# Kernel tuning notes

Measured on AMD Instinct MI355X. Metric: run time of the kernel, lower is better.

Reference implementation:

```python
import jax, jax.numpy as jnp
import numpy as np

N = 100000
M = 20000
NNZ = 1000000
D_IN = 128
D_OUT = 128


def setup_inputs() -> dict:
    key = jax.random.key(0)
    ks = jax.random.split(key, 6)
    return {
        "node_features": jax.random.normal(ks[0], (N, D_IN), dtype=jnp.float32),
        "data": jax.random.uniform(ks[1], (NNZ,), dtype=jnp.float32),
        "W": jax.random.normal(ks[2], (D_OUT, D_IN), dtype=jnp.float32) / np.sqrt(D_IN),
        "b": jax.random.normal(ks[3], (D_OUT,), dtype=jnp.float32),
        "v_idx": jax.random.randint(ks[4], (NNZ,), 0, N, dtype=jnp.int32),
        "e_idx": jax.random.randint(ks[5], (NNZ,), 0, M, dtype=jnp.int32),
        "n": N,
        "m": M,
    }


def reference(node_features, data, W, b, v_idx, e_idx, n, m):
    # Linear projection (eqx.nn.Linear: y = W @ x + b, vmapped over nodes)
    x = node_features @ W.T + b  # [n, d_out]

    # Degree normalization terms
    d_e = jax.ops.segment_sum(data, e_idx, num_segments=m)  # [m]
    d_v = jax.ops.segment_sum(data, v_idx, num_segments=n)  # [n]
    d_e_inv = jnp.where(d_e > 0, 1.0 / d_e, 0.0)
    d_v_inv = jnp.where(d_v > 0, 1.0 / d_v, 0.0)

    # vertex -> edge: H.T @ x via gather-scale-scatter
    e = jax.ops.segment_sum(x[v_idx] * data[:, None], e_idx, num_segments=m)  # [m, d_out]
    e = e * d_e_inv[:, None]

    # edge -> vertex: H @ e via gather-scale-scatter
    out = jax.ops.segment_sum(e[e_idx] * data[:, None], v_idx, num_segments=n)  # [n, d_out]
    out = out * d_v_inv[:, None]
    return out
```

## Files before the change

kernel.cpp:

```cpp
#include <hip/hip_runtime.h>

#define DF  128
#define NB  128
#define ME  20000
#define EW  10000
#define VW  16667
#define VP  3
#define VSPAN (2 * VW)

typedef float f32x2 __attribute__((ext_vector_type(2)));

__device__ __forceinline__ unsigned bf16rne(float f) {
    unsigned u = __float_as_uint(f);
    return (u + 0x7fffu + ((u >> 16) & 1u)) >> 16;
}

__device__ __forceinline__ unsigned w15enc(float f) {
    unsigned bits = __float_as_uint(f);
    unsigned r = (bits + 0xFFFu + ((bits >> 13) & 1u)) >> 13;
    return (r > (96u << 10)) ? (r - (96u << 10)) : 0u;
}
__device__ __forceinline__ float w15dec(unsigned w) {
    return w ? __uint_as_float((w + (96u << 10)) << 13) : 0.f;
}

#if __has_builtin(__builtin_amdgcn_fdot2_f32_bf16)
typedef __bf16 bf16x2 __attribute__((ext_vector_type(2)));
__device__ __forceinline__ float dot2bf(unsigned a, unsigned b, float c) {
    return __builtin_amdgcn_fdot2_f32_bf16(
        __builtin_bit_cast(bf16x2, a), __builtin_bit_cast(bf16x2, b), c, false);
}
#else
__device__ __forceinline__ float dot2bf(unsigned a, unsigned b, float c) {
    c += __uint_as_float(a << 16) * __uint_as_float(b << 16);
    c += __uint_as_float(a & 0xffff0000u) * __uint_as_float(b & 0xffff0000u);
    return c;
}
#endif

__global__ __launch_bounds__(256) void hist_lds(
    const int* __restrict__ vi, const int* __restrict__ ei,
    unsigned short* __restrict__ rankE, unsigned short* __restrict__ rankV,
    unsigned* __restrict__ bhE, unsigned* __restrict__ bhV, int nnz, int epb)
{
    __shared__ unsigned lh[VW];
    int b = blockIdx.x;
    int lo = b * epb;
    int hi = min(nnz, lo + epb);
    int iters = epb >> 10;

    for (int w = threadIdx.x; w < EW; w += 256) lh[w] = 0;
    __syncthreads();
    for (int it = 0; it < iters; ++it) {
        int i = lo + (it * 256 + threadIdx.x) * 4;
        if (i + 4 <= hi) {
            int4 e4 = *(const int4*)(ei + i);
            int ee[4] = {e4.x, e4.y, e4.z, e4.w};
            unsigned short r[4];
            #pragma unroll
            for (int q = 0; q < 4; ++q) {
                int sh = (ee[q] & 1) * 16;
                unsigned ret = atomicAdd(&lh[ee[q] >> 1], 1u << sh);
                r[q] = (unsigned short)((ret >> sh) & 0xffffu);
            }
            *(ushort4*)(rankE + i) = ushort4{r[0], r[1], r[2], r[3]};
        } else {
            for (int j = i; j < hi; ++j) {
                int e = ei[j]; int sh = (e & 1) * 16;
                unsigned ret = atomicAdd(&lh[e >> 1], 1u << sh);
                rankE[j] = (unsigned short)((ret >> sh) & 0xffffu);
            }
        }
    }
    __syncthreads();
    for (int w = threadIdx.x; w < EW; w += 256)
        bhE[(size_t)b * EW + w] = lh[w];

    for (int p = 0; p < VP; ++p) {
        int vbase = p * VSPAN;
        __syncthreads();
        for (int w = threadIdx.x; w < VW; w += 256) lh[w] = 0;
        __syncthreads();
        for (int it = 0; it < iters; ++it) {
            int i = lo + (it * 256 + threadIdx.x) * 4;
            if (i + 4 <= hi) {
                int4 v4 = *(const int4*)(vi + i);
                int vv[4] = {v4.x, v4.y, v4.z, v4.w};
                #pragma unroll
                for (int q = 0; q < 4; ++q) {
                    int d = vv[q] - vbase;
                    if (d >= 0 && d < VSPAN) {
                        int sh = (d & 1) * 16;
                        unsigned ret = atomicAdd(&lh[d >> 1], 1u << sh);
                        rankV[i + q] = (unsigned short)((ret >> sh) & 0xffffu);
                    }
                }
            } else {
                for (int j = i; j < hi; ++j) {
                    int d = vi[j] - vbase;
                    if (d >= 0 && d < VSPAN) {
                        int sh = (d & 1) * 16;
                        unsigned ret = atomicAdd(&lh[d >> 1], 1u << sh);
                        rankV[j] = (unsigned short)((ret >> sh) & 0xffffu);
                    }
                }
            }
        }
        __syncthreads();
        for (int w = threadIdx.x; w < VW; w += 256)
            bhV[(size_t)b * (VP * VW) + p * VW + w] = lh[w];
    }
}

__global__ __launch_bounds__(256) void scan_cols_conv(
    unsigned* __restrict__ bhE, unsigned* __restrict__ bhV,
    int* __restrict__ totE, int* __restrict__ totV,
    const float* __restrict__ nf, const float* __restrict__ W,
    unsigned* __restrict__ nfh, unsigned* __restrict__ wp, int n, int n64)
{
    int tid = blockIdx.x * 256 + threadIdx.x;
    if (tid < EW) {
        unsigned run0 = 0, run1 = 0;
        #pragma unroll 4
        for (int b = 0; b < NB; ++b) {
            unsigned w = bhE[(size_t)b * EW + tid];
            bhE[(size_t)b * EW + tid] = run0 | (run1 << 16);
            run0 += w & 0xffffu; run1 += w >> 16;
        }
        totE[2 * tid] = (int)run0;
        totE[2 * tid + 1] = (int)run1;
    } else if (tid < EW + VP * VW) {
        int w = tid - EW;
        unsigned run0 = 0, run1 = 0;
        #pragma unroll 4
        for (int b = 0; b < NB; ++b) {
            unsigned x = bhV[(size_t)b * (VP * VW) + w];
            bhV[(size_t)b * (VP * VW) + w] = run0 | (run1 << 16);
            run0 += x & 0xffffu; run1 += x >> 16;
        }
        int p = w / VW, wi = w - p * VW;
        int k0 = p * VSPAN + 2 * wi;
        if (k0 < n) totV[k0] = (int)run0;
        if (k0 + 1 < n) totV[k0 + 1] = (int)run1;
    }
    int nth = gridDim.x * 256;
    const float2* __restrict__ in2 = (const float2*)nf;
    for (int i = tid; i < n64; i += nth) {
        float2 f = in2[i];
        nfh[i] = bf16rne(f.x) | (bf16rne(f.y) << 16);
    }
    if (tid < DF * 64) {
        int j = tid >> 6, k2 = tid & 63;
        float2 f = ((const float2*)W)[tid];
        wp[k2 * DF + j] = bf16rne(f.x) | (bf16rne(f.y) << 16);
    }
}

__global__ __launch_bounds__(256) void scan_k1(
    const int* __restrict__ totE, const int* __restrict__ totV,
    int* __restrict__ bsum, int m, int len)
{
    __shared__ int s[256];
    int tid = threadIdx.x;
    int base = blockIdx.x * 2048 + tid * 8;
    int t = 0;
    #pragma unroll
    for (int i = 0; i < 8; ++i) {
        int idx = base + i;
        if (idx < len) t += (idx < m) ? totE[idx] : totV[idx - m];
    }
    s[tid] = t; __syncthreads();
    for (int d = 128; d > 0; d >>= 1) {
        if (tid < d) s[tid] += s[tid + d];
        __syncthreads();
    }
    if (tid == 0) bsum[blockIdx.x] = s[0];
}

__global__ __launch_bounds__(256) void scan_k2(int* __restrict__ bsum, int nb)
{
    __shared__ int s[256];
    int t = threadIdx.x;
    int v = (t < nb) ? bsum[t] : 0;
    s[t] = v; __syncthreads();
    for (int d = 1; d < 256; d <<= 1) {
        int u = (t >= d) ? s[t - d] : 0;
        __syncthreads();
        s[t] += u;
        __syncthreads();
    }
    if (t < nb) bsum[t] = s[t] - v;
}

__global__ __launch_bounds__(256) void scan_k3(
    const int* __restrict__ totE, const int* __restrict__ totV,
    const int* __restrict__ bsum, int* __restrict__ seg, int m, int len)
{
    __shared__ int s[256];
    int tid = threadIdx.x;
    int base = blockIdx.x * 2048 + tid * 8;
    int v[8]; int t = 0;
    #pragma unroll
    for (int i = 0; i < 8; ++i) {
        int idx = base + i;
        v[i] = (idx < len) ? ((idx < m) ? totE[idx] : totV[idx - m]) : 0;
        t += v[i];
    }
    s[tid] = t; __syncthreads();
    for (int d = 1; d < 256; d <<= 1) {
        int u = (tid >= d) ? s[tid - d] : 0;
        __syncthreads();
        s[tid] += u;
        __syncthreads();
    }
    int run = bsum[blockIdx.x] + (s[tid] - t);
    #pragma unroll
    for (int i = 0; i < 8; ++i) {
        int idx = base + i;
        if (idx < len) { seg[idx] = run; run += v[i]; }
    }
}

__global__ __launch_bounds__(256) void place_kernel(
    const int* __restrict__ vi, const int* __restrict__ ei,
    const float* __restrict__ data,
    const unsigned short* __restrict__ rankE,
    const unsigned short* __restrict__ rankV,
    const int* __restrict__ seg,
    const unsigned* __restrict__ bhE, const unsigned* __restrict__ bhV,
    unsigned* __restrict__ pair, int nnz, int m, int epb)
{
    int base = (blockIdx.x * 256 + threadIdx.x) * 4;
    if (base + 4 <= nnz) {
        int bH = base / epb;
        const unsigned* __restrict__ be = bhE + (size_t)bH * EW;
        const unsigned* __restrict__ bv = bhV + (size_t)bH * (VP * VW);
        int4 e4 = *(const int4*)(ei + base);
        int4 v4 = *(const int4*)(vi + base);
        ushort4 re4 = *(const ushort4*)(rankE + base);
        ushort4 rv4 = *(const ushort4*)(rankV + base);
        float4 d4 = *(const float4*)(data + base);
        int ee[4] = {e4.x, e4.y, e4.z, e4.w};
        int vv[4] = {v4.x, v4.y, v4.z, v4.w};
        unsigned short rre[4] = {re4.x, re4.y, re4.z, re4.w};
        unsigned short rrv[4] = {rv4.x, rv4.y, rv4.z, rv4.w};
        float dd[4] = {d4.x, d4.y, d4.z, d4.w};
        #pragma unroll
        for (int q = 0; q < 4; ++q) {
            unsigned w15 = w15enc(dd[q]) << 17;
            unsigned bwE = be[ee[q] >> 1];
            int baseE = (int)((bwE >> ((ee[q] & 1) * 16)) & 0xffffu);
            int p = vv[q] / VSPAN;
            int d = vv[q] - p * VSPAN;
            unsigned bwV = bv[p * VW + (d >> 1)];
            int baseV = (int)((bwV >> ((d & 1) * 16)) & 0xffffu);
            int pe = seg[ee[q]] + baseE + rre[q];
            int pv = seg[m + vv[q]] + baseV + rrv[q];
            __builtin_nontemporal_store(w15 | (unsigned)vv[q], pair + pe);
            __builtin_nontemporal_store(w15 | (unsigned)ee[q], pair + pv);
        }
    } else {
        for (int i = base; i < nnz; ++i) {
            int bH = i / epb;
            int e = ei[i], v = vi[i];
            unsigned w15 = w15enc(data[i]) << 17;
            unsigned bwE = bhE[(size_t)bH * EW + (e >> 1)];
            int baseE = (int)((bwE >> ((e & 1) * 16)) & 0xffffu);
            int p = v / VSPAN;
            int d = v - p * VSPAN;
            unsigned bwV = bhV[(size_t)bH * (VP * VW) + p * VW + (d >> 1)];
            int baseV = (int)((bwV >> ((d & 1) * 16)) & 0xffffu);
            int pe = seg[e] + baseE + rankE[i];
            int pv = seg[m + v] + baseV + rankV[i];
            __builtin_nontemporal_store(w15 | (unsigned)v, pair + pe);
            __builtin_nontemporal_store(w15 | (unsigned)e, pair + pv);
        }
    }
}

__global__ __launch_bounds__(256) void gather_y_linear(
    const unsigned* __restrict__ nfh, const int* __restrict__ seg,
    const unsigned* __restrict__ pair, const unsigned* __restrict__ wp,
    const float* __restrict__ b, unsigned* __restrict__ e16, int m)
{
    __shared__ unsigned rowbuf[4][64];
    int wv = threadIdx.x >> 6;
    int wid = (blockIdx.x * 256 + threadIdx.x) >> 6;
    int lane = threadIdx.x & 63;
    if (wid >= m) return;
    int start = seg[wid];
    int end   = seg[wid + 1];
    float ax = 0.f, ay = 0.f, ws = 0.f;
    int k = start;
    for (; k + 16 <= end; k += 16) {
        unsigned p[16];
        #pragma unroll
        for (int q = 0; q < 16; ++q) p[q] = __builtin_nontemporal_load(pair + k + q);
        unsigned u[16];
        #pragma unroll
        for (int q = 0; q < 16; ++q) u[q] = nfh[(size_t)(p[q] & 0x1FFFFu) * 64 + lane];
        #pragma unroll
        for (int q = 0; q < 16; ++q) {
            float w = w15dec(p[q] >> 17);
            ax += w * __uint_as_float(u[q] << 16);
            ay += w * __uint_as_float(u[q] & 0xffff0000u);
            ws += w;
        }
    }
    for (; k + 4 <= end; k += 4) {
        unsigned p[4];
        #pragma unroll
        for (int q = 0; q < 4; ++q) p[q] = __builtin_nontemporal_load(pair + k + q);
        unsigned u[4];
        #pragma unroll
        for (int q = 0; q < 4; ++q) u[q] = nfh[(size_t)(p[q] & 0x1FFFFu) * 64 + lane];
        #pragma unroll
        for (int q = 0; q < 4; ++q) {
            float w = w15dec(p[q] >> 17);
            ax += w * __uint_as_float(u[q] << 16);
            ay += w * __uint_as_float(u[q] & 0xffff0000u);
            ws += w;
        }
    }
    for (; k < end; ++k) {
        unsigned p0 = __builtin_nontemporal_load(pair + k);
        float w0 = w15dec(p0 >> 17);
        unsigned ua = nfh[(size_t)(p0 & 0x1FFFFu) * 64 + lane];
        ax += w0 * __uint_as_float(ua << 16);
        ay += w0 * __uint_as_float(ua & 0xffff0000u);
        ws += w0;
    }
    float inv = (ws > 0.f) ? 1.f / ws : 0.f;
    rowbuf[wv][lane] = bf16rne(ax * inv) | (bf16rne(ay * inv) << 16);

    float2 bb = ((const float2*)b)[lane];
    float acc0 = (ws > 0.f) ? bb.x : 0.f;
    float acc1 = (ws > 0.f) ? bb.y : 0.f;
    const unsigned* __restrict__ row = rowbuf[wv];
    #pragma unroll 8
    for (int k2 = 0; k2 < 64; ++k2) {
        unsigned r = row[k2];
        uint2 u = ((const uint2*)(wp + k2 * DF))[lane];
        acc0 = dot2bf(r, u.x, acc0);
        acc1 = dot2bf(r, u.y, acc1);
    }
    e16[(size_t)wid * 64 + lane] = bf16rne(acc0) | (bf16rne(acc1) << 16);
}

__global__ __launch_bounds__(256) void gather_out(
    const unsigned* __restrict__ e16, const int* __restrict__ seg,
    const unsigned* __restrict__ pair,
    float* __restrict__ out, int n, int m, int tot)
{
    int wid = (blockIdx.x * 256 + threadIdx.x) >> 6;
    int lane = threadIdx.x & 63;
    if (wid >= n) return;
    int idx = m + wid;
    int start = seg[idx];
    int end   = (wid == n - 1) ? tot : seg[idx + 1];
    float ax = 0.f, ay = 0.f, ws = 0.f;
    int k = start;
    for (; k + 16 <= end; k += 16) {
        unsigned p[16];
        #pragma unroll
        for (int q = 0; q < 16; ++q) p[q] = __builtin_nontemporal_load(pair + k + q);
        unsigned u[16];
        #pragma unroll
        for (int q = 0; q < 16; ++q) u[q] = e16[(size_t)(p[q] & 0x1FFFFu) * 64 + lane];
        #pragma unroll
        for (int q = 0; q < 16; ++q) {
            float w = w15dec(p[q] >> 17);
            ax += w * __uint_as_float(u[q] << 16);
            ay += w * __uint_as_float(u[q] & 0xffff0000u);
            ws += w;
        }
    }
    for (; k + 4 <= end; k += 4) {
        unsigned p[4];
        #pragma unroll
        for (int q = 0; q < 4; ++q) p[q] = __builtin_nontemporal_load(pair + k + q);
        unsigned u[4];
        #pragma unroll
        for (int q = 0; q < 4; ++q) u[q] = e16[(size_t)(p[q] & 0x1FFFFu) * 64 + lane];
        #pragma unroll
        for (int q = 0; q < 4; ++q) {
            float w = w15dec(p[q] >> 17);
            ax += w * __uint_as_float(u[q] << 16);
            ay += w * __uint_as_float(u[q] & 0xffff0000u);
            ws += w;
        }
    }
    for (; k < end; ++k) {
        unsigned p0 = __builtin_nontemporal_load(pair + k);
        float w0 = w15dec(p0 >> 17);
        unsigned ua = e16[(size_t)(p0 & 0x1FFFFu) * 64 + lane];
        ax += w0 * __uint_as_float(ua << 16);
        ay += w0 * __uint_as_float(ua & 0xffff0000u);
        ws += w0;
    }
    float inv = (ws > 0.f) ? 1.f / ws : 0.f;
    f32x2 o = {ax * inv, ay * inv};
    __builtin_nontemporal_store(o, (f32x2*)out + (size_t)wid * 64 + lane);
}

extern "C" void kernel_launch(void* const* d_in, const int* in_sizes, int n_in,
                              void* d_out, int out_size, void* d_ws, size_t ws_size,
                              hipStream_t stream)
{
    const float* nf   = (const float*)d_in[0];
    const float* data = (const float*)d_in[1];
    const float* W    = (const float*)d_in[2];
    const float* b    = (const float*)d_in[3];
    const int*   vi   = (const int*)d_in[4];
    const int*   ei   = (const int*)d_in[5];

    const int n   = in_sizes[0] / DF;
    const int nnz = in_sizes[1];
    const int m   = ME;

    const int epb = ((nnz + NB - 1) / NB + 1023) & ~1023;

    int*   seg   = (int*)d_ws;
    int*   bsum  = seg + (m + n);
    int*   totE  = bsum + 256;
    int*   totV  = totE + m;
    unsigned short* rankE = (unsigned short*)(totV + n);
    unsigned short* rankV = rankE + nnz;
    unsigned* e16 = (unsigned*)rankE;
    unsigned* pair = (unsigned*)rankE + ((size_t)m * 64 > (size_t)nnz ?
                     (size_t)m * 64 : (size_t)nnz);
    unsigned* wp  = pair + 2 * (size_t)nnz;
    unsigned* nfh = wp + DF * 64;
    unsigned* bhE = nfh + (size_t)n * 64;
    unsigned* bhV = bhE + (size_t)NB * EW;
    float* out   = (float*)d_out;

    hist_lds<<<NB, 256, 0, stream>>>(vi, ei, rankE, rankV, bhE, bhV, nnz, epb);

    scan_cols_conv<<<512, 256, 0, stream>>>(bhE, bhV, totE, totV,
                                            nf, W, nfh, wp, n, n * 64);

    int len = m + n;
    int nb = (len + 2047) / 2048;
    scan_k1<<<nb, 256, 0, stream>>>(totE, totV, bsum, m, len);
    scan_k2<<<1, 256, 0, stream>>>(bsum, nb);
    scan_k3<<<nb, 256, 0, stream>>>(totE, totV, bsum, seg, m, len);

    int nbQ = (nnz / 4 + 255) / 256;
    place_kernel<<<nbQ, 256, 0, stream>>>(vi, ei, data, rankE, rankV, seg,
                                          bhE, bhV, pair, nnz, m, epb);

    gather_y_linear<<<(m + 3) / 4, 256, 0, stream>>>(nfh, seg, pair, wp, b, e16, m);
    gather_out<<<(n + 3) / 4, 256, 0, stream>>>(e16, seg, pair, out, n, m, 2 * nnz);
}
```

Baseline: 269.0 us.

## Split scatter placement into binned staging pass plus windowed write pass

Replaces the single random-scatter placement kernel with two passes. The first bins each edge's two destination positions into 8K-entry windows per block, using an LDS histogram and scan, and writes (position, payload) records to a staging buffer that reuses the output allocation. The second pass has one block per window replay the records, so writes into pair land in a local address range. The aim is to turn fully random global stores into localized ones, at the cost of recomputing positions twice, doubling the traffic through the 64-bit staging buffer, and running only 128 blocks in the first pass.

After: 377.6 us. 1.4x slower.

```diff
diff --git a/kernel.cpp b/kernel.cpp
--- a/kernel.cpp
+++ b/kernel.cpp
@@ -7,8 +7,12 @@
 #define VW  16667
 #define VP  3
 #define VSPAN (2 * VW)
+#define WINB 256
+#define WSH  13
+#define RPB  16384
 
 typedef float f32x2 __attribute__((ext_vector_type(2)));
+typedef unsigned long long ull;
 
 __device__ __forceinline__ unsigned bf16rne(float f) {
     unsigned u = __float_as_uint(f);
@@ -221,59 +225,91 @@
     }
 }
 
-__global__ __launch_bounds__(256) void place_kernel(
+__device__ __forceinline__ void edge_pos(
+    int i, int e, int v, const int* __restrict__ seg,
+    const unsigned* __restrict__ be, const unsigned* __restrict__ bv,
+    const unsigned short* __restrict__ rankE,
+    const unsigned short* __restrict__ rankV,
+    int m, int* pe, int* pv)
+{
+    unsigned bwE = be[e >> 1];
+    int baseE = (int)((bwE >> ((e & 1) * 16)) & 0xffffu);
+    int p = v / VSPAN;
+    int d = v - p * VSPAN;
+    unsigned bwV = bv[p * VW + (d >> 1)];
+    int baseV = (int)((bwV >> ((d & 1) * 16)) & 0xffffu);
+    *pe = seg[e] + baseE + rankE[i];
+    *pv = seg[m + v] + baseV + rankV[i];
+}
+
+__global__ __launch_bounds__(256) void place_a(
     const int* __restrict__ vi, const int* __restrict__ ei,
     const float* __restrict__ data,
     const unsigned short* __restrict__ rankE,
     const unsigned short* __restrict__ rankV,
     const int* __restrict__ seg,
     const unsigned* __restrict__ bhE, const unsigned* __restrict__ bhV,
-    unsigned* __restrict__ pair, int nnz, int m, int epb)
-{
-    int base = (blockIdx.x * 256 + threadIdx.x) * 4;
-    if (base + 4 <= nnz) {
-        int bH = base / epb;
-        const unsigned* __restrict__ be = bhE + (size_t)bH * EW;
-        const unsigned* __restrict__ bv = bhV + (size_t)bH * (VP * VW);
-        int4 e4 = *(const int4*)(ei + base);
-        int4 v4 = *(const int4*)(vi + base);
-        ushort4 re4 = *(const ushort4*)(rankE + base);
-        ushort4 rv4 = *(const ushort4*)(rankV + base);
-        float4 d4 = *(const float4*)(data + base);
-        int ee[4] = {e4.x, e4.y, e4.z, e4.w};
-        int vv[4] = {v4.x, v4.y, v4.z, v4.w};
-        unsigned short rre[4] = {re4.x, re4.y, re4.z, re4.w};
-        unsigned short rrv[4] = {rv4.x, rv4.y, rv4.z, rv4.w};
-        float dd[4] = {d4.x, d4.y, d4.z, d4.w};
-        #pragma unroll
-        for (int q = 0; q < 4; ++q) {
-            unsigned w15 = w15enc(dd[q]) << 17;
-            unsigned bwE = be[ee[q] >> 1];
-            int baseE = (int)((bwE >> ((ee[q] & 1) * 16)) & 0xffffu);
-            int p = vv[q] / VSPAN;
-            int d = vv[q] - p * VSPAN;
-            unsigned bwV = bv[p * VW + (d >> 1)];
-            int baseV = (int)((bwV >> ((d & 1) * 16)) & 0xffffu);
-            int pe = seg[ee[q]] + baseE + rre[q];
-            int pv = seg[m + vv[q]] + baseV + rrv[q];
-            __builtin_nontemporal_store(w15 | (unsigned)vv[q], pair + pe);
-            __builtin_nontemporal_store(w15 | (unsigned)ee[q], pair + pv);
-        }
-    } else {
-        for (int i = base; i < nnz; ++i) {
-            int bH = i / epb;
-            int e = ei[i], v = vi[i];
-            unsigned w15 = w15enc(data[i]) << 17;
-            unsigned bwE = bhE[(size_t)bH * EW + (e >> 1)];
-            int baseE = (int)((bwE >> ((e & 1) * 16)) & 0xffffu);
-            int p = v / VSPAN;
-            int d = v - p * VSPAN;
-            unsigned bwV = bhV[(size_t)bH * (VP * VW) + p * VW + (d >> 1)];
-            int baseV = (int)((bwV >> ((d & 1) * 16)) & 0xffffu);
-            int pe = seg[e] + baseE + rankE[i];
-            int pv = seg[m + v] + baseV + rankV[i];
-            __builtin_nontemporal_store(w15 | (unsigned)v, pair + pe);
-            __builtin_nontemporal_store(w15 | (unsigned)e, pair + pv);
+    ull* __restrict__ stage, unsigned* __restrict__ tstart,
+    unsigned* __restrict__ tcnt, int nnz, int m, int epb)
+{
+    __shared__ unsigned cnt[WINB];
+    __shared__ unsigned off[WINB];
+    __shared__ unsigned s[WINB];
+    int b = blockIdx.x;
+    int lo = b * epb;
+    int hi = min(nnz, lo + epb);
+    const unsigned* __restrict__ be = bhE + (size_t)b * EW;
+    const unsigned* __restrict__ bv = bhV + (size_t)b * (VP * VW);
+
+    for (int w = threadIdx.x; w < WINB; w += 256) cnt[w] = 0;
+    __syncthreads();
+
+    for (int i = lo + threadIdx.x; i < hi; i += 256) {
+        int e = ei[i], v = vi[i], pe, pv;
+        edge_pos(i, e, v, seg, be, bv, rankE, rankV, m, &pe, &pv);
+        atomicAdd(&cnt[pe >> WSH], 1u);
+        atomicAdd(&cnt[pv >> WSH], 1u);
+    }
+    __syncthreads();
+
+    int t = threadIdx.x;
+    unsigned c = cnt[t];
+    tcnt[(size_t)b * WINB + t] = c;
+    s[t] = c; __syncthreads();
+    for (int d = 1; d < 256; d <<= 1) {
+        unsigned u = (t >= d) ? s[t - d] : 0;
+        __syncthreads();
+        s[t] += u;
+        __syncthreads();
+    }
+    off[t] = s[t] - c;
+    tstart[(size_t)b * WINB + t] = s[t] - c;
+    __syncthreads();
+
+    ull* __restrict__ sb = stage + (size_t)b * RPB;
+    for (int i = lo + threadIdx.x; i < hi; i += 256) {
+        int e = ei[i], v = vi[i], pe, pv;
+        edge_pos(i, e, v, seg, be, bv, rankE, rankV, m, &pe, &pv);
+        unsigned w15 = w15enc(data[i]) << 17;
+        unsigned oe = atomicAdd(&off[pe >> WSH], 1u);
+        sb[oe] = ((ull)(unsigned)pe << 32) | (w15 | (unsigned)v);
+        unsigned ov = atomicAdd(&off[pv >> WSH], 1u);
+        sb[ov] = ((ull)(unsigned)pv << 32) | (w15 | (unsigned)e);
+    }
+}
+
+__global__ __launch_bounds__(256) void place_b(
+    const ull* __restrict__ stage, const unsigned* __restrict__ tstart,
+    const unsigned* __restrict__ tcnt, unsigned* __restrict__ pair)
+{
+    int w = blockIdx.x;
+    for (int b = 0; b < NB; ++b) {
+        unsigned st = tstart[(size_t)b * WINB + w];
+        unsigned c  = tcnt[(size_t)b * WINB + w];
+        const ull* __restrict__ src = stage + (size_t)b * RPB + st;
+        for (unsigned r = threadIdx.x; r < c; r += 256) {
+            ull rec = __builtin_nontemporal_load(src + r);
+            pair[(unsigned)(rec >> 32)] = (unsigned)rec;
         }
     }
 }
@@ -433,7 +469,10 @@
     unsigned* nfh = wp + DF * 64;
     unsigned* bhE = nfh + (size_t)n * 64;
     unsigned* bhV = bhE + (size_t)NB * EW;
+    unsigned* tstart = bhV + (size_t)NB * (VP * VW);
+    unsigned* tcnt   = tstart + (size_t)NB * WINB;
     float* out   = (float*)d_out;
+    ull* stage = (ull*)d_out;
 
     hist_lds<<<NB, 256, 0, stream>>>(vi, ei, rankE, rankV, bhE, bhV, nnz, epb);
 
@@ -446,9 +485,9 @@
     scan_k2<<<1, 256, 0, stream>>>(bsum, nb);
     scan_k3<<<nb, 256, 0, stream>>>(totE, totV, bsum, seg, m, len);
 
-    int nbQ = (nnz / 4 + 255) / 256;
-    place_kernel<<<nbQ, 256, 0, stream>>>(vi, ei, data, rankE, rankV, seg,
-                                          bhE, bhV, pair, nnz, m, epb);
+    place_a<<<NB, 256, 0, stream>>>(vi, ei, data, rankE, rankV, seg,
+                                    bhE, bhV, stage, tstart, tcnt, nnz, m, epb);
+    place_b<<<WINB, 256, 0, stream>>>(stage, tstart, tcnt, pair);
 
     gather_y_linear<<<(m + 3) / 4, 256, 0, stream>>>(nfh, seg, pair, wp, b, e16, m);
     gather_out<<<(n + 3) / 4, 256, 0, stream>>>(e16, seg, pair, out, n, m, 2 * nnz);
```
